# Optimization experiments

Hardware: AMD Instinct MI355X
Metric: run time of the kernel (lower is better)

Reference implementation:

```python
import jax, jax.numpy as jnp
import numpy as np

KH, KW, STRIDE = 5, 5, 1
RY, RX = 60, 60  # (64-5)/1+1


def setup_inputs() -> dict:
    key = jax.random.key(0)
    k1, k2, k3 = jax.random.split(key, 3)
    x = jax.random.normal(k1, (128, 3, 64, 64), dtype=jnp.float32)
    # per-position unshared weights, fan-in = C*KH*KW = 75, flatten order (C, kh, kw)
    W = jax.random.normal(k2, (RY, RX, 32, 75), dtype=jnp.float32) * (1.0 / np.sqrt(75.0))
    b = jax.random.normal(k3, (RY, RX, 32), dtype=jnp.float32) * 0.01
    return {"x": x, "W": W, "b": b}


def _extract_patches(x):
    # x: [B, C, H, W] -> patches [B, RY, RX, C*KH*KW], flatten order (C, kh, kw)
    slices = []
    for dy in range(KH):
        for dx in range(KW):
            slices.append(x[:, :, dy:dy + (RY - 1) * STRIDE + 1:STRIDE,
                              dx:dx + (RX - 1) * STRIDE + 1:STRIDE])  # [B, C, RY, RX]
    p = jnp.stack(slices, axis=2)                 # [B, C, KH*KW, RY, RX]
    p = p.transpose(0, 3, 4, 1, 2)                # [B, RY, RX, C, KH*KW]
    return p.reshape(p.shape[0], RY, RX, -1)      # [B, RY, RX, C*KH*KW]


def reference(x, W, b):
    patches = _extract_patches(x)                       # [B, RY, RX, K]
    # per-position linear: out[b,o,y,x] = sum_k patches[b,y,x,k] * W[y,x,o,k] + b[y,x,o]
    out = jnp.einsum('byxk,yxok->byxo', patches, W) + b  # [B, RY, RX, O]
    return out.transpose(0, 3, 1, 2)                     # [B, O, RY, RX]
```

## Files before the change

kernel.cpp:

```cpp
#include <hip/hip_runtime.h>
#include <hip/hip_bf16.h>


#define RY 60
#define RX 60
#define OC 32
#define BATCH 128
#define CIN 3
#define HW 64

typedef __attribute__((ext_vector_type(8))) short short8;
typedef __attribute__((ext_vector_type(4))) float f32x4;

__device__ __forceinline__ ushort bf16u(float f) {
    __hip_bfloat16 h = __float2bfloat16(f);
    return *reinterpret_cast<ushort*>(&h);
}
__device__ __forceinline__ unsigned pk2(float a, float b) {
    return (unsigned)bf16u(a) | ((unsigned)bf16u(b) << 16);
}

__global__ __launch_bounds__(256, 4) void lc2d_fused(
    const float* __restrict__ x, const float* __restrict__ w,
    const float* __restrict__ bias, float* __restrict__ out)
{
    __shared__ __align__(16) float wlds[4 * 2400 + 128];

    const int tid = threadIdx.x;
    const int id  = blockIdx.x;
    const int lin = (id & 7) * 450 + (id >> 3);
    const int bs  = lin & 3;
    const int pg  = lin >> 2;
    const int y   = pg / 15;
    const int grp = pg - y * 15;
    const int x0  = grp * 4;
    const int pos0 = y * RX + x0;

    const int lane = tid & 63;
    const int wid  = tid >> 6;
    const int lrow = lane & 15;
    const int lgrp = lane >> 4;
    const int mt   = wid >> 1;
    const int nt   = wid & 1;
    const int bbase = bs * 32 + mt * 16;
    const int o     = nt * 16 + lrow;

    float4 av[4][2];
    #pragma unroll
    for (int ks = 0; ks < 4; ++ks) {
        const int cm = ks * 4 + lgrp;
        if (cm < 15) {
            const int c  = cm / 5;
            const int kh = cm - c * 5;
            const int b  = bbase + lrow;
            const float* src = x + (size_t)((b * CIN + c) * HW + (y + kh)) * HW + x0;
            av[ks][0] = *(const float4*)(src);
            av[ks][1] = *(const float4*)(src + 4);
        }
    }

    {
        const float* gW = w + (size_t)pos0 * 2400;
        for (int j = wid; j < 38; j += 4) {
            const int chunk0 = j * 64;
            int ci = chunk0 + lane;
            if (ci > 2399) ci = 2399;
            __builtin_amdgcn_global_load_lds(
                (const __attribute__((address_space(1))) unsigned*)(gW + ci * 4),
                (__attribute__((address_space(3))) unsigned*)&wlds[chunk0 * 4],
                16, 0, 0);
        }
    }

    float bv[4];
    #pragma unroll
    for (int xi = 0; xi < 4; ++xi)
        bv[xi] = bias[(size_t)(pos0 + xi) * OC + o];

    short8 af[4];
    #pragma unroll
    for (int ks = 0; ks < 4; ++ks) {
        const int cm = ks * 4 + lgrp;
        union { unsigned u[4]; short8 s8; } cv;
        if (cm < 15) {
            cv.u[0] = pk2(av[ks][0].x, av[ks][0].y);
            cv.u[1] = pk2(av[ks][0].z, av[ks][0].w);
            cv.u[2] = pk2(av[ks][1].x, av[ks][1].y);
            cv.u[3] = pk2(av[ks][1].z, av[ks][1].w);
        } else {
            cv.u[0] = 0u; cv.u[1] = 0u; cv.u[2] = 0u; cv.u[3] = 0u;
        }
        af[ks] = cv.s8;
    }

    __syncthreads();

    f32x4 accx[4];
    #pragma unroll
    for (int xi = 0; xi < 4; ++xi) accx[xi] = (f32x4){0.f, 0.f, 0.f, 0.f};

    const int wbase = o * 75;
    #pragma unroll
    for (int ks = 0; ks < 4; ++ks) {
        const int cm = ks * 4 + lgrp;
        const int soff = wbase + cm * 5;
        #pragma unroll
        for (int xi = 0; xi < 4; ++xi) {
            const float* s = &wlds[xi * 2400 + soff];
            const ushort h[5] = {bf16u(s[0]), bf16u(s[1]), bf16u(s[2]),
                                 bf16u(s[3]), bf16u(s[4])};
            unsigned wd[4] = {0u, 0u, 0u, 0u};
            #pragma unroll
            for (int kw = 0; kw < 5; ++kw) {
                const int ws = xi + kw;
                wd[ws >> 1] |= (unsigned)h[kw] << ((ws & 1) * 16);
            }
            union { unsigned u[4]; short8 s8; } cv;
            cv.u[0] = wd[0]; cv.u[1] = wd[1]; cv.u[2] = wd[2]; cv.u[3] = wd[3];
            accx[xi] = __builtin_amdgcn_mfma_f32_16x16x32_bf16(af[ks], cv.s8, accx[xi], 0, 0, 0);
        }
    }

    #pragma unroll
    for (int r = 0; r < 4; ++r) {
        const int bg = bbase + lgrp * 4 + r;
        float4 v;
        v.x = accx[0][r] + bv[0];
        v.y = accx[1][r] + bv[1];
        v.z = accx[2][r] + bv[2];
        v.w = accx[3][r] + bv[3];
        *(float4*)(out + (size_t)(bg * OC + o) * (RY * RX) + pos0) = v;
    }
}

extern "C" void kernel_launch(void* const* d_in, const int* in_sizes, int n_in,
                              void* d_out, int out_size, void* d_ws, size_t ws_size,
                              hipStream_t stream) {
    const float* x    = (const float*)d_in[0];
    const float* w    = (const float*)d_in[1];
    const float* bias = (const float*)d_in[2];
    float* out        = (float*)d_out;
    lc2d_fused<<<3600, 256, 0, stream>>>(x, w, bias, out);
}
```

Before: 42.83 us.

## Split weight packing into a pre-pass kernel and fold bias into the MFMA

A first kernel converts the per-position weights to bf16, stored already shifted into the banded MFMA B-fragment layout in workspace memory, with the bias placed in the padding K slot. The main kernel then loads those fragments straight from global memory, with no LDS and no per-use conversion. A constant 1.0 in the A operand adds the bias inside the MFMA. Each block now processes 4 position groups, so there are fewer, larger blocks. The cost is an extra launch and a round-trip through a roughly 29 MB bf16 workspace, and the bias is rounded to bf16. When the workspace is too small, the original kernel is kept as a fallback.

```diff
diff --git a/kernel.cpp b/kernel.cpp
--- a/kernel.cpp
+++ b/kernel.cpp
@@ -8,9 +8,12 @@
 #define BATCH 128
 #define CIN 3
 #define HW 64
+#define NPOS 3600
+#define KPACK 128
 
 typedef __attribute__((ext_vector_type(8))) short short8;
 typedef __attribute__((ext_vector_type(4))) float f32x4;
+typedef unsigned long long ull;
 
 __device__ __forceinline__ ushort bf16u(float f) {
     __hip_bfloat16 h = __float2bfloat16(f);
@@ -19,46 +22,171 @@
 __device__ __forceinline__ unsigned pk2(float a, float b) {
     return (unsigned)bf16u(a) | ((unsigned)bf16u(b) << 16);
 }
-
-__global__ __launch_bounds__(256, 4) void lc2d_fused(
+__device__ __forceinline__ int swz900(int id) {
+    const int xcd = id & 7, ii = id >> 3;
+    return (xcd < 4 ? xcd * 113 : 452 + (xcd - 4) * 112) + ii;
+}
+
+__global__ __launch_bounds__(256, 4) void lc2d_wpack(
+    const float* __restrict__ w, const float* __restrict__ bias,
+    ushort* __restrict__ wp)
+{
+    __shared__ __align__(16) float wlds[9600 + 128];
+
+    const int G   = swz900(blockIdx.x);
+    const int tid = threadIdx.x;
+    const int lane = tid & 63, wid = tid >> 6;
+
+    {
+        const float* gW = w + (size_t)G * 4 * (OC * 75);
+        for (int j = wid; j < 38; j += 4) {
+            const int chunk0 = j * 64;
+            int ci = chunk0 + lane;
+            if (ci > 2399) ci = 2399;
+            __builtin_amdgcn_global_load_lds(
+                (const __attribute__((address_space(1))) unsigned*)(gW + ci * 4),
+                (__attribute__((address_space(3))) unsigned*)&wlds[chunk0 * 4],
+                16, 0, 0);
+        }
+    }
+
+    const int xi = tid >> 6, o = (tid >> 1) & 31, half = tid & 1;
+    const float bv = bias[(size_t)(G * 4 + xi) * OC + o];
+    __syncthreads();
+
+    const float* src = &wlds[xi * 2400 + o * 75];
+    const int s = xi * 16;
+    unsigned wd[32];
+    #pragma unroll
+    for (int i = 0; i < 32; ++i) wd[i] = 0u;
+
+    #pragma unroll
+    for (int cc = 0; cc < 8; ++cc) {
+        const int cm = half * 8 + cc;
+        if (cm < 15) {
+            const float* sp = src + cm * 5;
+            const ushort h0 = bf16u(sp[0]), h1 = bf16u(sp[1]), h2 = bf16u(sp[2]),
+                         h3 = bf16u(sp[3]), h4 = bf16u(sp[4]);
+            const ull lo = (ull)h0 | ((ull)h1 << 16) | ((ull)h2 << 32) | ((ull)h3 << 48);
+            const ull hi = (ull)h4;
+            const ull rlo = lo << s;
+            const ull rhi = (hi << s) | (s ? (lo >> (64 - s)) : 0ull);
+            wd[cc * 4 + 0] = (unsigned)rlo;
+            wd[cc * 4 + 1] = (unsigned)(rlo >> 32);
+            wd[cc * 4 + 2] = (unsigned)rhi;
+            wd[cc * 4 + 3] = (unsigned)(rhi >> 32);
+        } else {
+            wd[cc * 4 + 0] = (unsigned)bf16u(bv);
+        }
+    }
+    ushort* dst = wp + ((size_t)(G * 4 + xi) * OC + o) * KPACK + half * 64;
+    #pragma unroll
+    for (int q = 0; q < 8; ++q)
+        *reinterpret_cast<uint4*>(dst + q * 8) =
+            make_uint4(wd[q * 4], wd[q * 4 + 1], wd[q * 4 + 2], wd[q * 4 + 3]);
+}
+
+__global__ __launch_bounds__(256, 2) void lc2d_main(
+    const float* __restrict__ x, const ushort* __restrict__ wp,
+    float* __restrict__ out)
+{
+    const int lin = swz900(blockIdx.x);
+    const int bs = lin & 3;
+    const int q  = lin >> 2;
+
+    const int lane = threadIdx.x & 63, wid = threadIdx.x >> 6;
+    const int lrow = lane & 15, lgrp = lane >> 4;
+    const int mt = wid >> 1, nt = wid & 1;
+    const int bbase = bs * 32 + mt * 16;
+    const int o = nt * 16 + lrow;
+    const int b = bbase + lrow;
+
+    f32x4 linebuf[4][4];
+
+    #pragma unroll
+    for (int j = 0; j < 4; ++j) {
+        const int G   = q * 4 + j;
+        const int y   = G / 15;
+        const int x0  = (G - y * 15) * 4;
+
+        short8 af[4];
+        #pragma unroll
+        for (int ks = 0; ks < 4; ++ks) {
+            const int cm = ks * 4 + lgrp;
+            union { unsigned u[4]; short8 s8; } cv;
+            if (cm < 15) {
+                const int c = cm / 5, kh = cm - c * 5;
+                const float* src = x + (size_t)((b * CIN + c) * HW + (y + kh)) * HW + x0;
+                const float4 v0 = *(const float4*)(src);
+                const float4 v1 = *(const float4*)(src + 4);
+                cv.u[0] = pk2(v0.x, v0.y); cv.u[1] = pk2(v0.z, v0.w);
+                cv.u[2] = pk2(v1.x, v1.y); cv.u[3] = pk2(v1.z, v1.w);
+            } else {
+                cv.u[0] = 0x3f80u; cv.u[1] = 0u; cv.u[2] = 0u; cv.u[3] = 0u;
+            }
+            af[ks] = cv.s8;
+        }
+
+        f32x4 accx[4];
+        #pragma unroll
+        for (int xi = 0; xi < 4; ++xi) accx[xi] = (f32x4){0.f, 0.f, 0.f, 0.f};
+
+        #pragma unroll
+        for (int xi = 0; xi < 4; ++xi) {
+            const ushort* wb = wp + ((size_t)(4 * G + xi) * OC + o) * KPACK + lgrp * 8;
+            #pragma unroll
+            for (int ks = 0; ks < 4; ++ks) {
+                const short8 bf = *(const short8*)(wb + ks * 32);
+                accx[xi] = __builtin_amdgcn_mfma_f32_16x16x32_bf16(af[ks], bf, accx[xi], 0, 0, 0);
+            }
+        }
+
+        #pragma unroll
+        for (int r = 0; r < 4; ++r)
+            linebuf[j][r] = (f32x4){accx[0][r], accx[1][r], accx[2][r], accx[3][r]};
+    }
+
+    const int bg0 = bbase + lgrp * 4;
+    #pragma unroll
+    for (int r = 0; r < 4; ++r) {
+        float* ob = out + (size_t)((bg0 + r) * OC + o) * NPOS + 16 * q;
+        #pragma unroll
+        for (int j = 0; j < 4; ++j)
+            *reinterpret_cast<f32x4*>(ob + 4 * j) = linebuf[j][r];
+    }
+}
+
+__global__ __launch_bounds__(256, 4) void lc2d_fb(
     const float* __restrict__ x, const float* __restrict__ w,
     const float* __restrict__ bias, float* __restrict__ out)
 {
     __shared__ __align__(16) float wlds[4 * 2400 + 128];
-
     const int tid = threadIdx.x;
     const int id  = blockIdx.x;
     const int lin = (id & 7) * 450 + (id >> 3);
     const int bs  = lin & 3;
     const int pg  = lin >> 2;
     const int y   = pg / 15;
-    const int grp = pg - y * 15;
-    const int x0  = grp * 4;
+    const int x0  = (pg - y * 15) * 4;
     const int pos0 = y * RX + x0;
-
-    const int lane = tid & 63;
-    const int wid  = tid >> 6;
-    const int lrow = lane & 15;
-    const int lgrp = lane >> 4;
-    const int mt   = wid >> 1;
-    const int nt   = wid & 1;
+    const int lane = tid & 63, wid = tid >> 6;
+    const int lrow = lane & 15, lgrp = lane >> 4;
+    const int mt = wid >> 1, nt = wid & 1;
     const int bbase = bs * 32 + mt * 16;
-    const int o     = nt * 16 + lrow;
+    const int o = nt * 16 + lrow;
 
     float4 av[4][2];
     #pragma unroll
     for (int ks = 0; ks < 4; ++ks) {
         const int cm = ks * 4 + lgrp;
         if (cm < 15) {
-            const int c  = cm / 5;
-            const int kh = cm - c * 5;
-            const int b  = bbase + lrow;
+            const int c = cm / 5, kh = cm - c * 5;
+            const int b = bbase + lrow;
             const float* src = x + (size_t)((b * CIN + c) * HW + (y + kh)) * HW + x0;
             av[ks][0] = *(const float4*)(src);
             av[ks][1] = *(const float4*)(src + 4);
         }
     }
-
     {
         const float* gW = w + (size_t)pos0 * 2400;
         for (int j = wid; j < 38; j += 4) {
@@ -71,11 +199,9 @@
                 16, 0, 0);
         }
     }
-
     float bv[4];
     #pragma unroll
-    for (int xi = 0; xi < 4; ++xi)
-        bv[xi] = bias[(size_t)(pos0 + xi) * OC + o];
+    for (int xi = 0; xi < 4; ++xi) bv[xi] = bias[(size_t)(pos0 + xi) * OC + o];
 
     short8 af[4];
     #pragma unroll
@@ -83,22 +209,16 @@
         const int cm = ks * 4 + lgrp;
         union { unsigned u[4]; short8 s8; } cv;
         if (cm < 15) {
-            cv.u[0] = pk2(av[ks][0].x, av[ks][0].y);
-            cv.u[1] = pk2(av[ks][0].z, av[ks][0].w);
-            cv.u[2] = pk2(av[ks][1].x, av[ks][1].y);
-            cv.u[3] = pk2(av[ks][1].z, av[ks][1].w);
-        } else {
-            cv.u[0] = 0u; cv.u[1] = 0u; cv.u[2] = 0u; cv.u[3] = 0u;
-        }
+            cv.u[0] = pk2(av[ks][0].x, av[ks][0].y); cv.u[1] = pk2(av[ks][0].z, av[ks][0].w);
+            cv.u[2] = pk2(av[ks][1].x, av[ks][1].y); cv.u[3] = pk2(av[ks][1].z, av[ks][1].w);
+        } else { cv.u[0] = cv.u[1] = cv.u[2] = cv.u[3] = 0u; }
         af[ks] = cv.s8;
     }
-
     __syncthreads();
 
     f32x4 accx[4];
     #pragma unroll
     for (int xi = 0; xi < 4; ++xi) accx[xi] = (f32x4){0.f, 0.f, 0.f, 0.f};
-
     const int wbase = o * 75;
     #pragma unroll
     for (int ks = 0; ks < 4; ++ks) {
@@ -107,8 +227,7 @@
         #pragma unroll
         for (int xi = 0; xi < 4; ++xi) {
             const float* s = &wlds[xi * 2400 + soff];
-            const ushort h[5] = {bf16u(s[0]), bf16u(s[1]), bf16u(s[2]),
-                                 bf16u(s[3]), bf16u(s[4])};
+            const ushort h[5] = {bf16u(s[0]), bf16u(s[1]), bf16u(s[2]), bf16u(s[3]), bf16u(s[4])};
             unsigned wd[4] = {0u, 0u, 0u, 0u};
             #pragma unroll
             for (int kw = 0; kw < 5; ++kw) {
@@ -120,15 +239,12 @@
             accx[xi] = __builtin_amdgcn_mfma_f32_16x16x32_bf16(af[ks], cv.s8, accx[xi], 0, 0, 0);
         }
     }
-
     #pragma unroll
     for (int r = 0; r < 4; ++r) {
         const int bg = bbase + lgrp * 4 + r;
         float4 v;
-        v.x = accx[0][r] + bv[0];
-        v.y = accx[1][r] + bv[1];
-        v.z = accx[2][r] + bv[2];
-        v.w = accx[3][r] + bv[3];
+        v.x = accx[0][r] + bv[0]; v.y = accx[1][r] + bv[1];
+        v.z = accx[2][r] + bv[2]; v.w = accx[3][r] + bv[3];
         *(float4*)(out + (size_t)(bg * OC + o) * (RY * RX) + pos0) = v;
     }
 }
@@ -140,5 +256,13 @@
     const float* w    = (const float*)d_in[1];
     const float* bias = (const float*)d_in[2];
     float* out        = (float*)d_out;
-    lc2d_fused<<<3600, 256, 0, stream>>>(x, w, bias, out);
-}
+
+    const size_t wp_bytes = (size_t)NPOS * OC * KPACK * sizeof(ushort);
+    if (ws_size >= wp_bytes) {
+        ushort* wp = (ushort*)d_ws;
+        lc2d_wpack<<<900, 256, 0, stream>>>(w, bias, wp);
+        lc2d_main<<<900, 256, 0, stream>>>(x, wp, out);
+    } else {
+        lc2d_fb<<<3600, 256, 0, stream>>>(x, w, bias, out);
+    }
+}
```

After: 80.82 us. +88.7%, slower.
